# Optimization experiments

Hardware: AMD Instinct MI355X
Metric: run time of the kernel (lower is better)

The kernel has to match this reference:

```python
import jax, jax.numpy as jnp
import numpy as np

N_NODES = 50000
N_EDGES = 800000
IN_CH = 128
HID = 128


def setup_inputs() -> dict:
    key = jax.random.key(0)
    ks = jax.random.split(key, 16)
    inp = {
        "x": jax.random.normal(ks[0], (N_NODES, IN_CH), dtype=jnp.float32),
        "edge_index": jax.random.randint(ks[1], (2, N_EDGES), 0, N_NODES, dtype=jnp.int64),
        "batch_size": 1024,
    }
    dims = [(IN_CH, HID), (HID, HID), (HID, HID)]
    for i, (din, dout) in enumerate(dims):
        s = 1.0 / np.sqrt(din)
        inp[f"W_l{i}"] = jax.random.uniform(ks[2 + 4 * i], (dout, din), jnp.float32, -s, s)
        inp[f"b_l{i}"] = jax.random.uniform(ks[3 + 4 * i], (dout,), jnp.float32, -s, s)
        inp[f"W_r{i}"] = jax.random.uniform(ks[4 + 4 * i], (dout, din), jnp.float32, -s, s)
        inp[f"a{i}"] = jnp.full((dout,), 0.25, dtype=jnp.float32)  # PReLU slope
    return inp


def _sage_prelu(x, src, dst, W_l, b_l, W_r, a):
    # mean aggregation of source messages at target nodes
    msg_sum = jax.ops.segment_sum(x[src], dst, num_segments=N_NODES)  # [N, din]
    deg = jax.ops.segment_sum(jnp.ones((src.shape[0],), x.dtype), dst, num_segments=N_NODES)
    agg = msg_sum / jnp.maximum(deg, 1.0)[:, None]
    out = agg @ W_l.T + b_l + x @ W_r.T  # lin_l(aggr) + lin_r(x), bias on lin_l only
    return jnp.where(out > 0, out, a * out)  # per-channel PReLU


def reference(x, edge_index, batch_size, W_l0, b_l0, W_r0, a0, W_l1, b_l1, W_r1, a1, W_l2, b_l2, W_r2, a2):
    src, dst = edge_index[0], edge_index[1]
    x = _sage_prelu(x, src, dst, W_l0, b_l0, W_r0, a0)
    x = _sage_prelu(x, src, dst, W_l1, b_l1, W_r1, a1)
    x = _sage_prelu(x, src, dst, W_l2, b_l2, W_r2, a2)
    return x[:batch_size]
```

## Files before the change

### kernel.cpp

```cpp
#include <hip/hip_runtime.h>

#define NN 50000
#define NE 800000
#define C 128
#define SCAN_BLOCKS ((NN + 255) / 256)
#define EB2 ((NE / 2 + 255) / 256)
#define SPLITB 1563
#define WB 96
#define EB4 ((NE / 4 + 255) / 256)
#define ASTRIDE 136

typedef __attribute__((ext_vector_type(8))) short bf16x8;
typedef __attribute__((ext_vector_type(4))) float f32x4;
typedef unsigned short ushort;

__device__ inline ushort bf16_rn(float f) {
    unsigned u = __builtin_bit_cast(unsigned, f);
    u += 0x7FFF + ((u >> 16) & 1);
    return (ushort)(u >> 16);
}
__device__ inline void split_bf16(float f, ushort& hi, ushort& lo) {
    hi = bf16_rn(f);
    float hif = __builtin_bit_cast(float, (unsigned)hi << 16);
    lo = bf16_rn(f - hif);
}
__device__ inline float bf_lo(unsigned u) { return __builtin_bit_cast(float, u << 16); }
__device__ inline float bf_hi(unsigned u) { return __builtin_bit_cast(float, u & 0xFFFF0000u); }


__global__ __launch_bounds__(256)
void prep_kernel(const int* __restrict__ dst, const float* __restrict__ x,
                 const float* __restrict__ W0, const float* __restrict__ W1,
                 const float* __restrict__ W2, const float* __restrict__ W3,
                 const float* __restrict__ W4, const float* __restrict__ W5,
                 int* __restrict__ deg, int* __restrict__ pos,
                 ushort* __restrict__ Ah, ushort* __restrict__ Al,
                 ushort* __restrict__ Wh, ushort* __restrict__ Wl) {
    int t = threadIdx.x;
    if (blockIdx.x < EB2) {
        int e0 = (blockIdx.x * 256 + t) * 2;
        if (e0 < NE) {
            int2 d2 = *(const int2*)(dst + e0);
            int p0 = atomicAdd(&deg[d2.x], 1);
            int p1 = atomicAdd(&deg[d2.y], 1);
            *(int2*)(pos + e0) = make_int2(p0, p1);
        }
    } else if (blockIdx.x < EB2 + SPLITB) {
        int tid = (blockIdx.x - EB2) * 256 + t;
        const int total = NN * C / 4;
        for (int i = tid; i < total; i += SPLITB * 256) {
            f32x4 v = ((const f32x4*)x)[i];
            ushort h0, h1, h2, h3, l0, l1, l2, l3;
            split_bf16(v.x, h0, l0);
            split_bf16(v.y, h1, l1);
            split_bf16(v.z, h2, l2);
            split_bf16(v.w, h3, l3);
            *(uint2*)(Ah + (size_t)i * 4) = make_uint2((unsigned)h0 | ((unsigned)h1 << 16),
                                                       (unsigned)h2 | ((unsigned)h3 << 16));
            *(uint2*)(Al + (size_t)i * 4) = make_uint2((unsigned)l0 | ((unsigned)l1 << 16),
                                                       (unsigned)l2 | ((unsigned)l3 << 16));
        }
    } else {
        const float* Ws[6] = {W0, W1, W2, W3, W4, W5};
        int i = (blockIdx.x - EB2 - SPLITB) * 256 + t;
        int mat = i >> 12;
        f32x4 v = ((const f32x4*)Ws[mat])[i & 4095];
        ushort h0, h1, h2, h3, l0, l1, l2, l3;
        split_bf16(v.x, h0, l0);
        split_bf16(v.y, h1, l1);
        split_bf16(v.z, h2, l2);
        split_bf16(v.w, h3, l3);
        *(uint2*)(Wh + (size_t)i * 4) = make_uint2((unsigned)h0 | ((unsigned)h1 << 16),
                                                   (unsigned)h2 | ((unsigned)h3 << 16));
        *(uint2*)(Wl + (size_t)i * 4) = make_uint2((unsigned)l0 | ((unsigned)l1 << 16),
                                                   (unsigned)l2 | ((unsigned)l3 << 16));
    }
}


__global__ __launch_bounds__(256)
void scan1_kernel(const int* __restrict__ deg, int* __restrict__ row_ptr,
                  int* __restrict__ bsum) {
    __shared__ int wsum[4];
    __shared__ int wpre[4];
    int t = threadIdx.x, lane = t & 63, w = t >> 6;
    int i = blockIdx.x * 256 + t;
    int v = (i < NN) ? deg[i] : 0;
    int s = v;
    #pragma unroll
    for (int off = 1; off < 64; off <<= 1) {
        int y = __shfl_up(s, off, 64);
        if (lane >= off) s += y;
    }
    if (lane == 63) wsum[w] = s;
    __syncthreads();
    if (t == 0) {
        int acc = 0;
        #pragma unroll
        for (int j = 0; j < 4; ++j) { wpre[j] = acc; acc += wsum[j]; }
        bsum[blockIdx.x] = acc;
    }
    __syncthreads();
    if (i <= NN) row_ptr[i] = wpre[w] + (s - v);
}


__global__ __launch_bounds__(256)
void scan2_kernel(const int* __restrict__ bsum, int* __restrict__ boff) {
    __shared__ int wsum[4];
    __shared__ int wpre[4];
    int t = threadIdx.x, lane = t & 63, w = t >> 6;
    int v = (t < SCAN_BLOCKS) ? bsum[t] : 0;
    int s = v;
    #pragma unroll
    for (int off = 1; off < 64; off <<= 1) {
        int y = __shfl_up(s, off, 64);
        if (lane >= off) s += y;
    }
    if (lane == 63) wsum[w] = s;
    __syncthreads();
    if (t == 0) {
        int acc = 0;
        #pragma unroll
        for (int j = 0; j < 4; ++j) { wpre[j] = acc; acc += wsum[j]; }
    }
    __syncthreads();
    if (t < SCAN_BLOCKS) boff[t] = wpre[w] + (s - v);
}


__global__ __launch_bounds__(256)
void fill2_kernel(const int* __restrict__ src, const int* __restrict__ dst,
                  const int* __restrict__ row_ptr, const int* __restrict__ boff,
                  const int* __restrict__ pos, int* __restrict__ col) {
    int e0 = (blockIdx.x * 256 + threadIdx.x) * 4;
    if (e0 >= NE) return;
    int4 da = *(const int4*)(dst + e0);
    int4 sa = *(const int4*)(src + e0);
    int4 pa = *(const int4*)(pos + e0);
    col[row_ptr[da.x] + boff[da.x >> 8] + pa.x] = sa.x;
    col[row_ptr[da.y] + boff[da.y >> 8] + pa.y] = sa.y;
    col[row_ptr[da.z] + boff[da.z >> 8] + pa.z] = sa.z;
    col[row_ptr[da.w] + boff[da.w >> 8] + pa.w] = sa.w;
}


__global__ __launch_bounds__(256)
void agg_kernel(const ushort* __restrict__ xh, const int* __restrict__ row_ptr,
                const int* __restrict__ boff, const int* __restrict__ col,
                ushort* __restrict__ aggh, ushort* __restrict__ aggl, int nodes) {
    int node = (blockIdx.x * blockDim.x + threadIdx.x) >> 6;
    int lane = threadIdx.x & 63;
    if (node >= nodes) return;
    int quad = lane >> 4;
    int ql   = lane & 15;
    int start = row_ptr[node] + boff[node >> 8];
    int end   = row_ptr[node + 1] + boff[(node + 1) >> 8];
    const uint4* xr = (const uint4*)xh;
    float a0=0,a1=0,a2=0,a3=0,a4=0,a5=0,a6=0,a7=0;
    int e = start;
    for (; e + 7 < end; e += 8) {
        int i0 = col[e + quad];
        int i1 = col[e + 4 + quad];
        uint4 u0 = xr[(size_t)i0 * 16 + ql];
        uint4 u1 = xr[(size_t)i1 * 16 + ql];
        a0 += bf_lo(u0.x) + bf_lo(u1.x); a1 += bf_hi(u0.x) + bf_hi(u1.x);
        a2 += bf_lo(u0.y) + bf_lo(u1.y); a3 += bf_hi(u0.y) + bf_hi(u1.y);
        a4 += bf_lo(u0.z) + bf_lo(u1.z); a5 += bf_hi(u0.z) + bf_hi(u1.z);
        a6 += bf_lo(u0.w) + bf_lo(u1.w); a7 += bf_hi(u0.w) + bf_hi(u1.w);
    }
    for (; e + 3 < end; e += 4) {
        uint4 u = xr[(size_t)col[e + quad] * 16 + ql];
        a0 += bf_lo(u.x); a1 += bf_hi(u.x);
        a2 += bf_lo(u.y); a3 += bf_hi(u.y);
        a4 += bf_lo(u.z); a5 += bf_hi(u.z);
        a6 += bf_lo(u.w); a7 += bf_hi(u.w);
    }
    int rem = end - e;
    if (quad < rem) {
        uint4 u = xr[(size_t)col[e + quad] * 16 + ql];
        a0 += bf_lo(u.x); a1 += bf_hi(u.x);
        a2 += bf_lo(u.y); a3 += bf_hi(u.y);
        a4 += bf_lo(u.z); a5 += bf_hi(u.z);
        a6 += bf_lo(u.w); a7 += bf_hi(u.w);
    }
    a0 += __shfl_xor(a0, 16, 64); a0 += __shfl_xor(a0, 32, 64);
    a1 += __shfl_xor(a1, 16, 64); a1 += __shfl_xor(a1, 32, 64);
    a2 += __shfl_xor(a2, 16, 64); a2 += __shfl_xor(a2, 32, 64);
    a3 += __shfl_xor(a3, 16, 64); a3 += __shfl_xor(a3, 32, 64);
    a4 += __shfl_xor(a4, 16, 64); a4 += __shfl_xor(a4, 32, 64);
    a5 += __shfl_xor(a5, 16, 64); a5 += __shfl_xor(a5, 32, 64);
    a6 += __shfl_xor(a6, 16, 64); a6 += __shfl_xor(a6, 32, 64);
    a7 += __shfl_xor(a7, 16, 64); a7 += __shfl_xor(a7, 32, 64);
    if (quad == 0) {
        float inv = 1.0f / (float)max(end - start, 1);
        float m[8] = {a0*inv, a1*inv, a2*inv, a3*inv, a4*inv, a5*inv, a6*inv, a7*inv};
        ushort h[8], o[8];
        #pragma unroll
        for (int j = 0; j < 8; ++j) split_bf16(m[j], h[j], o[j]);
        size_t off = (size_t)node * C + ql * 8;
        *(uint4*)(aggh + off) = make_uint4((unsigned)h[0] | ((unsigned)h[1] << 16),
                                           (unsigned)h[2] | ((unsigned)h[3] << 16),
                                           (unsigned)h[4] | ((unsigned)h[5] << 16),
                                           (unsigned)h[6] | ((unsigned)h[7] << 16));
        *(uint4*)(aggl + off) = make_uint4((unsigned)o[0] | ((unsigned)o[1] << 16),
                                           (unsigned)o[2] | ((unsigned)o[3] << 16),
                                           (unsigned)o[4] | ((unsigned)o[5] << 16),
                                           (unsigned)o[6] | ((unsigned)o[7] << 16));
    }
}


__global__ __launch_bounds__(256, 3)
void gemm_kernel(const ushort* __restrict__ Ah, const ushort* __restrict__ Al,
                 const ushort* __restrict__ Xh, const ushort* __restrict__ Xl,
                 const ushort* __restrict__ Wlh, const ushort* __restrict__ Wll,
                 const ushort* __restrict__ Wrh, const ushort* __restrict__ Wrl,
                 const float* __restrict__ bl, const float* __restrict__ slope,
                 float* __restrict__ outf, ushort* __restrict__ outh,
                 ushort* __restrict__ outl, int rows) {
    __shared__ ushort Ahi[64 * ASTRIDE];
    __shared__ ushort Alo[64 * ASTRIDE];
    int t = threadIdx.x;
    int lane = t & 63;
    int w = t >> 6;
    int l = lane & 15;
    int q = lane >> 4;
    int row0 = blockIdx.x * 64;

    f32x4 acc[4][2];
    #pragma unroll
    for (int mt = 0; mt < 4; ++mt)
        #pragma unroll
        for (int nt = 0; nt < 2; ++nt)
            acc[mt][nt] = (f32x4){0.f, 0.f, 0.f, 0.f};

    #pragma unroll
    for (int mat = 0; mat < 2; ++mat) {
        const ushort* WH = mat ? Wrh : Wlh;
        const ushort* WL = mat ? Wrl : Wll;
        const ushort* Ph = mat ? Xh : Ah;
        const ushort* Pl = mat ? Xl : Al;

        bf16x8 bhi[2][4], blo[2][4];
        #pragma unroll
        for (int nt = 0; nt < 2; ++nt) {
            int n = w * 32 + nt * 16 + l;
            const ushort* wp = WH + (size_t)n * C + q * 8;
            const ushort* wq = WL + (size_t)n * C + q * 8;
            #pragma unroll
            for (int kb = 0; kb < 4; ++kb) {
                bhi[nt][kb] = *(const bf16x8*)(wp + kb * 32);
                blo[nt][kb] = *(const bf16x8*)(wq + kb * 32);
            }
        }

        __syncthreads();
        int ar = t >> 2;
        int aq = t & 3;
        int r = min(row0 + ar, rows - 1);
        ushort* dh = Ahi + ar * ASTRIDE + aq * 32;
        ushort* dl = Alo + ar * ASTRIDE + aq * 32;
        const ushort* ph = Ph + (size_t)r * C + aq * 32;
        const ushort* pl = Pl + (size_t)r * C + aq * 32;
        #pragma unroll
        for (int i = 0; i < 4; ++i) {
            *(uint4*)(dh + i * 8) = *(const uint4*)(ph + i * 8);
            *(uint4*)(dl + i * 8) = *(const uint4*)(pl + i * 8);
        }
        __syncthreads();

        #pragma unroll
        for (int kb = 0; kb < 4; ++kb) {
            #pragma unroll
            for (int mt = 0; mt < 4; ++mt) {
                int off = (mt * 16 + l) * ASTRIDE + kb * 32 + q * 8;
                bf16x8 ahi = *(const bf16x8*)(Ahi + off);
                bf16x8 alo = *(const bf16x8*)(Alo + off);
                #pragma unroll
                for (int nt = 0; nt < 2; ++nt) {
                    acc[mt][nt] = __builtin_amdgcn_mfma_f32_16x16x32_bf16(ahi, bhi[nt][kb], acc[mt][nt], 0, 0, 0);
                    acc[mt][nt] = __builtin_amdgcn_mfma_f32_16x16x32_bf16(alo, bhi[nt][kb], acc[mt][nt], 0, 0, 0);
                    acc[mt][nt] = __builtin_amdgcn_mfma_f32_16x16x32_bf16(ahi, blo[nt][kb], acc[mt][nt], 0, 0, 0);
                }
            }
        }
    }

    #pragma unroll
    for (int nt = 0; nt < 2; ++nt) {
        int n = w * 32 + nt * 16 + l;
        float b = bl[n], s = slope[n];
        #pragma unroll
        for (int mt = 0; mt < 4; ++mt) {
            #pragma unroll
            for (int rg = 0; rg < 4; ++rg) {
                int r = row0 + mt * 16 + q * 4 + rg;
                if (r < rows) {
                    float v = acc[mt][nt][rg] + b;
                    v = v > 0.f ? v : s * v;
                    if (outf) {
                        outf[(size_t)r * C + n] = v;
                    } else {
                        ushort hh, ll;
                        split_bf16(v, hh, ll);
                        outh[(size_t)r * C + n] = hh;
                        outl[(size_t)r * C + n] = ll;
                    }
                }
            }
        }
    }
}


extern "C" void kernel_launch(void* const* d_in, const int* in_sizes, int n_in,
                              void* d_out, int out_size, void* d_ws, size_t ws_size,
                              hipStream_t stream) {
    const float* x   = (const float*)d_in[0];
    const int*   src = (const int*)d_in[1];
    const int*   dst = src + NE;
    const float* Wl[3] = {(const float*)d_in[3], (const float*)d_in[7],  (const float*)d_in[11]};
    const float* bl[3] = {(const float*)d_in[4], (const float*)d_in[8],  (const float*)d_in[12]};
    const float* Wr[3] = {(const float*)d_in[5], (const float*)d_in[9],  (const float*)d_in[13]};
    const float* sl[3] = {(const float*)d_in[6], (const float*)d_in[10], (const float*)d_in[14]};

    int*   deg     = (int*)d_ws;
    int*   row_ptr = deg + 50016;
    int*   col     = row_ptr + 50016;
    int*   pos     = col + 800000;
    int*   bsum    = pos + 800000;
    int*   boff    = bsum + 256;
    ushort* Whs    = (ushort*)(boff + 256);
    ushort* Wls    = Whs + 6 * 16384;
    ushort* Gh     = Wls + 6 * 16384;
    ushort* Gl     = Gh + (size_t)NN * C;
    ushort* Ah     = Gl + (size_t)NN * C;
    ushort* Al     = Ah + (size_t)NN * C;
    ushort* Bh     = Al + (size_t)NN * C;
    ushort* Bl     = Bh + (size_t)NN * C;

    hipMemsetAsync(deg, 0, 50016 * sizeof(int), stream);

    prep_kernel<<<EB2 + SPLITB + WB, 256, 0, stream>>>(
        dst, x, Wl[0], Wr[0], Wl[1], Wr[1], Wl[2], Wr[2],
        deg, pos, Ah, Al, Whs, Wls);
    scan1_kernel<<<SCAN_BLOCKS, 256, 0, stream>>>(deg, row_ptr, bsum);
    scan2_kernel<<<1, 256, 0, stream>>>(bsum, boff);
    fill2_kernel<<<EB4, 256, 0, stream>>>(src, dst, row_ptr, boff, pos, col);

    int rows_out = out_size / C;

    agg_kernel<<<(NN + 3) / 4, 256, 0, stream>>>(Ah, row_ptr, boff, col, Gh, Gl, NN);
    gemm_kernel<<<(NN + 63) / 64, 256, 0, stream>>>(Gh, Gl, Ah, Al,
                                                    Whs + 0 * 16384, Wls + 0 * 16384,
                                                    Whs + 1 * 16384, Wls + 1 * 16384,
                                                    bl[0], sl[0], nullptr, Bh, Bl, NN);

    agg_kernel<<<(NN + 3) / 4, 256, 0, stream>>>(Bh, row_ptr, boff, col, Gh, Gl, NN);
    gemm_kernel<<<(NN + 63) / 64, 256, 0, stream>>>(Gh, Gl, Bh, Bl,
                                                    Whs + 2 * 16384, Wls + 2 * 16384,
                                                    Whs + 3 * 16384, Wls + 3 * 16384,
                                                    bl[1], sl[1], nullptr, Ah, Al, NN);

    agg_kernel<<<(rows_out + 3) / 4, 256, 0, stream>>>(Ah, row_ptr, boff, col, Gh, Gl, rows_out);
    gemm_kernel<<<(rows_out + 63) / 64, 256, 0, stream>>>(Gh, Gl, Ah, Al,
                                                          Whs + 4 * 16384, Wls + 4 * 16384,
                                                          Whs + 5 * 16384, Wls + 5 * 16384,
                                                          bl[2], sl[2], (float*)d_out, nullptr, nullptr,
                                                          rows_out);
}
```

Baseline: 301.8 us.

## Slice node features into four 32-channel planes for cache-friendly aggregation

Stores the bf16 hi/lo feature arrays in four channel-slice planes of 32 channels each (node-major within a slice), rather than row-major over all 128 channels. The aggregation kernel now gives each wave one slice, with half a wave per node and eight edges in parallel, so each gather pass touches a smaller working set that fits better in L2. The GEMM load and store paths are rewritten to match the sliced layout. The trade-off is that the column index list is read four times, and each gathered row segment is only 64 bytes.

```diff
diff --git a/kernel.cpp b/kernel.cpp
--- a/kernel.cpp
+++ b/kernel.cpp
@@ -3,6 +3,7 @@
 #define NN 50000
 #define NE 800000
 #define C 128
+#define SL (NN * 32)
 #define SCAN_BLOCKS ((NN + 255) / 256)
 #define EB2 ((NE / 2 + 255) / 256)
 #define SPLITB 1563
@@ -50,15 +51,19 @@
         const int total = NN * C / 4;
         for (int i = tid; i < total; i += SPLITB * 256) {
             f32x4 v = ((const f32x4*)x)[i];
+            int node = i >> 5;
+            int c4 = i & 31;
+            int s = c4 >> 3;
+            size_t o = (size_t)s * SL + (size_t)node * 32 + (c4 & 7) * 4;
             ushort h0, h1, h2, h3, l0, l1, l2, l3;
             split_bf16(v.x, h0, l0);
             split_bf16(v.y, h1, l1);
             split_bf16(v.z, h2, l2);
             split_bf16(v.w, h3, l3);
-            *(uint2*)(Ah + (size_t)i * 4) = make_uint2((unsigned)h0 | ((unsigned)h1 << 16),
-                                                       (unsigned)h2 | ((unsigned)h3 << 16));
-            *(uint2*)(Al + (size_t)i * 4) = make_uint2((unsigned)l0 | ((unsigned)l1 << 16),
-                                                       (unsigned)l2 | ((unsigned)l3 << 16));
+            *(uint2*)(Ah + o) = make_uint2((unsigned)h0 | ((unsigned)h1 << 16),
+                                           (unsigned)h2 | ((unsigned)h3 << 16));
+            *(uint2*)(Al + o) = make_uint2((unsigned)l0 | ((unsigned)l1 << 16),
+                                           (unsigned)l2 | ((unsigned)l3 << 16));
         }
     } else {
         const float* Ws[6] = {W0, W1, W2, W3, W4, W5};
@@ -146,67 +151,69 @@
 
 
 __global__ __launch_bounds__(256)
-void agg_kernel(const ushort* __restrict__ xh, const int* __restrict__ row_ptr,
+void agg_kernel(const ushort* __restrict__ xs, const int* __restrict__ row_ptr,
                 const int* __restrict__ boff, const int* __restrict__ col,
-                ushort* __restrict__ aggh, ushort* __restrict__ aggl, int nodes) {
-    int node = (blockIdx.x * blockDim.x + threadIdx.x) >> 6;
+                ushort* __restrict__ gh, ushort* __restrict__ gl, int nodes) {
+    int npw = (nodes + 1) >> 1;
+    int wid = blockIdx.x * 4 + (threadIdx.x >> 6);
+    if (wid >= 4 * npw) return;
+    int s = wid / npw;
+    int wp = wid - s * npw;
     int lane = threadIdx.x & 63;
+    int nh = lane >> 5;
+    int l32 = lane & 31;
+    int g = l32 >> 2;
+    int cl = l32 & 3;
+    int node = wp * 2 + nh;
     if (node >= nodes) return;
-    int quad = lane >> 4;
-    int ql   = lane & 15;
     int start = row_ptr[node] + boff[node >> 8];
     int end   = row_ptr[node + 1] + boff[(node + 1) >> 8];
-    const uint4* xr = (const uint4*)xh;
+    const ushort* xb = xs + (size_t)s * SL;
     float a0=0,a1=0,a2=0,a3=0,a4=0,a5=0,a6=0,a7=0;
     int e = start;
     for (; e + 7 < end; e += 8) {
-        int i0 = col[e + quad];
-        int i1 = col[e + 4 + quad];
-        uint4 u0 = xr[(size_t)i0 * 16 + ql];
-        uint4 u1 = xr[(size_t)i1 * 16 + ql];
-        a0 += bf_lo(u0.x) + bf_lo(u1.x); a1 += bf_hi(u0.x) + bf_hi(u1.x);
-        a2 += bf_lo(u0.y) + bf_lo(u1.y); a3 += bf_hi(u0.y) + bf_hi(u1.y);
-        a4 += bf_lo(u0.z) + bf_lo(u1.z); a5 += bf_hi(u0.z) + bf_hi(u1.z);
-        a6 += bf_lo(u0.w) + bf_lo(u1.w); a7 += bf_hi(u0.w) + bf_hi(u1.w);
-    }
-    for (; e + 3 < end; e += 4) {
-        uint4 u = xr[(size_t)col[e + quad] * 16 + ql];
+        int si = col[e + g];
+        uint4 u = *(const uint4*)(xb + (size_t)si * 32 + cl * 8);
         a0 += bf_lo(u.x); a1 += bf_hi(u.x);
         a2 += bf_lo(u.y); a3 += bf_hi(u.y);
         a4 += bf_lo(u.z); a5 += bf_hi(u.z);
         a6 += bf_lo(u.w); a7 += bf_hi(u.w);
     }
     int rem = end - e;
-    if (quad < rem) {
-        uint4 u = xr[(size_t)col[e + quad] * 16 + ql];
+    if (g < rem) {
+        int si = col[e + g];
+        uint4 u = *(const uint4*)(xb + (size_t)si * 32 + cl * 8);
         a0 += bf_lo(u.x); a1 += bf_hi(u.x);
         a2 += bf_lo(u.y); a3 += bf_hi(u.y);
         a4 += bf_lo(u.z); a5 += bf_hi(u.z);
         a6 += bf_lo(u.w); a7 += bf_hi(u.w);
     }
-    a0 += __shfl_xor(a0, 16, 64); a0 += __shfl_xor(a0, 32, 64);
-    a1 += __shfl_xor(a1, 16, 64); a1 += __shfl_xor(a1, 32, 64);
-    a2 += __shfl_xor(a2, 16, 64); a2 += __shfl_xor(a2, 32, 64);
-    a3 += __shfl_xor(a3, 16, 64); a3 += __shfl_xor(a3, 32, 64);
-    a4 += __shfl_xor(a4, 16, 64); a4 += __shfl_xor(a4, 32, 64);
-    a5 += __shfl_xor(a5, 16, 64); a5 += __shfl_xor(a5, 32, 64);
-    a6 += __shfl_xor(a6, 16, 64); a6 += __shfl_xor(a6, 32, 64);
-    a7 += __shfl_xor(a7, 16, 64); a7 += __shfl_xor(a7, 32, 64);
-    if (quad == 0) {
+    #pragma unroll
+    for (int off = 4; off <= 16; off <<= 1) {
+        a0 += __shfl_xor(a0, off, 64);
+        a1 += __shfl_xor(a1, off, 64);
+        a2 += __shfl_xor(a2, off, 64);
+        a3 += __shfl_xor(a3, off, 64);
+        a4 += __shfl_xor(a4, off, 64);
+        a5 += __shfl_xor(a5, off, 64);
+        a6 += __shfl_xor(a6, off, 64);
+        a7 += __shfl_xor(a7, off, 64);
+    }
+    if (g == 0) {
         float inv = 1.0f / (float)max(end - start, 1);
         float m[8] = {a0*inv, a1*inv, a2*inv, a3*inv, a4*inv, a5*inv, a6*inv, a7*inv};
         ushort h[8], o[8];
         #pragma unroll
         for (int j = 0; j < 8; ++j) split_bf16(m[j], h[j], o[j]);
-        size_t off = (size_t)node * C + ql * 8;
-        *(uint4*)(aggh + off) = make_uint4((unsigned)h[0] | ((unsigned)h[1] << 16),
-                                           (unsigned)h[2] | ((unsigned)h[3] << 16),
-                                           (unsigned)h[4] | ((unsigned)h[5] << 16),
-                                           (unsigned)h[6] | ((unsigned)h[7] << 16));
-        *(uint4*)(aggl + off) = make_uint4((unsigned)o[0] | ((unsigned)o[1] << 16),
-                                           (unsigned)o[2] | ((unsigned)o[3] << 16),
-                                           (unsigned)o[4] | ((unsigned)o[5] << 16),
-                                           (unsigned)o[6] | ((unsigned)o[7] << 16));
+        size_t off = (size_t)s * SL + (size_t)node * 32 + cl * 8;
+        *(uint4*)(gh + off) = make_uint4((unsigned)h[0] | ((unsigned)h[1] << 16),
+                                         (unsigned)h[2] | ((unsigned)h[3] << 16),
+                                         (unsigned)h[4] | ((unsigned)h[5] << 16),
+                                         (unsigned)h[6] | ((unsigned)h[7] << 16));
+        *(uint4*)(gl + off) = make_uint4((unsigned)o[0] | ((unsigned)o[1] << 16),
+                                         (unsigned)o[2] | ((unsigned)o[3] << 16),
+                                         (unsigned)o[4] | ((unsigned)o[5] << 16),
+                                         (unsigned)o[6] | ((unsigned)o[7] << 16));
     }
 }
 
@@ -261,8 +268,8 @@
         int r = min(row0 + ar, rows - 1);
         ushort* dh = Ahi + ar * ASTRIDE + aq * 32;
         ushort* dl = Alo + ar * ASTRIDE + aq * 32;
-        const ushort* ph = Ph + (size_t)r * C + aq * 32;
-        const ushort* pl = Pl + (size_t)r * C + aq * 32;
+        const ushort* ph = Ph + (size_t)aq * SL + (size_t)r * 32;
+        const ushort* pl = Pl + (size_t)aq * SL + (size_t)r * 32;
         #pragma unroll
         for (int i = 0; i < 4; ++i) {
             *(uint4*)(dh + i * 8) = *(const uint4*)(ph + i * 8);
@@ -304,8 +311,9 @@
                     } else {
                         ushort hh, ll;
                         split_bf16(v, hh, ll);
-                        outh[(size_t)r * C + n] = hh;
-                        outl[(size_t)r * C + n] = ll;
+                        size_t o = (size_t)w * SL + (size_t)r * 32 + nt * 16 + l;
+                        outh[o] = hh;
+                        outl[o] = ll;
                     }
                 }
             }
@@ -351,19 +359,20 @@
 
     int rows_out = out_size / C;
 
-    agg_kernel<<<(NN + 3) / 4, 256, 0, stream>>>(Ah, row_ptr, boff, col, Gh, Gl, NN);
+    agg_kernel<<<(4 * ((NN + 1) / 2) + 3) / 4, 256, 0, stream>>>(Ah, row_ptr, boff, col, Gh, Gl, NN);
     gemm_kernel<<<(NN + 63) / 64, 256, 0, stream>>>(Gh, Gl, Ah, Al,
                                                     Whs + 0 * 16384, Wls + 0 * 16384,
                                                     Whs + 1 * 16384, Wls + 1 * 16384,
                                                     bl[0], sl[0], nullptr, Bh, Bl, NN);
 
-    agg_kernel<<<(NN + 3) / 4, 256, 0, stream>>>(Bh, row_ptr, boff, col, Gh, Gl, NN);
+    agg_kernel<<<(4 * ((NN + 1) / 2) + 3) / 4, 256, 0, stream>>>(Bh, row_ptr, boff, col, Gh, Gl, NN);
     gemm_kernel<<<(NN + 63) / 64, 256, 0, stream>>>(Gh, Gl, Bh, Bl,
                                                     Whs + 2 * 16384, Wls + 2 * 16384,
                                                     Whs + 3 * 16384, Wls + 3 * 16384,
                                                     bl[1], sl[1], nullptr, Ah, Al, NN);
 
-    agg_kernel<<<(rows_out + 3) / 4, 256, 0, stream>>>(Ah, row_ptr, boff, col, Gh, Gl, rows_out);
+    agg_kernel<<<(4 * ((rows_out + 1) / 2) + 3) / 4, 256, 0, stream>>>(Ah, row_ptr, boff, col,
+                                                                      Gh, Gl, rows_out);
     gemm_kernel<<<(rows_out + 63) / 64, 256, 0, stream>>>(Gh, Gl, Ah, Al,
                                                           Whs + 4 * 16384, Wls + 4 * 16384,
                                                           Whs + 5 * 16384, Wls + 5 * 16384,
```

Measured after the change: 342.4 us. 1.13x slower.
